# Optimization experiments

Hardware: AMD Instinct MI355X
Metric: run time of the kernel (lower is better)

## Reference

```python
import jax, jax.numpy as jnp
import numpy as np

EMBED_DIM = 1024
ATTEN_DIM = 64


def setup_inputs() -> dict:
    key = jax.random.key(0)
    k_x, k_q, k_k, k_v = jax.random.split(key, 4)
    B, S = 4, 4096
    scale = 1.0 / np.sqrt(EMBED_DIM)
    x = jax.random.normal(k_x, (B, S, EMBED_DIM), dtype=jnp.float32)
    # torch nn.Linear weights are [out_features, in_features]
    Wq = jax.random.normal(k_q, (ATTEN_DIM, EMBED_DIM), dtype=jnp.float32) * scale
    Wk = jax.random.normal(k_k, (ATTEN_DIM, EMBED_DIM), dtype=jnp.float32) * scale
    Wv = jax.random.normal(k_v, (ATTEN_DIM, EMBED_DIM), dtype=jnp.float32) * scale
    return {"x": x, "Wq": Wq, "Wk": Wk, "Wv": Wv}


def reference(x, Wq, Wk, Wv):
    # q, k, v: [B, S, D]
    q = jnp.einsum('bse,de->bsd', x, Wq)
    k = jnp.einsum('bse,de->bsd', x, Wk)
    v = jnp.einsum('bse,de->bsd', x, Wv)
    d = k.shape[-1]
    scores = jnp.einsum('bsd,btd->bst', q, k) / jnp.sqrt(jnp.float32(d))
    S = x.shape[1]
    causal = jnp.tril(jnp.ones((S, S), dtype=bool))
    scores = jnp.where(causal[None, :, :], scores, -jnp.inf)
    attn = jax.nn.softmax(scores, axis=-1)
    return jnp.einsum('bst,btd->bsd', attn, v)
```

## Files before the change

### kernel.cpp

```cpp
#include <hip/hip_runtime.h>
#include <hip/hip_bf16.h>
#include <stdint.h>

typedef __attribute__((ext_vector_type(8))) short  short8;
typedef __attribute__((ext_vector_type(4))) short  short4v;
typedef __attribute__((ext_vector_type(4))) float  float4v;

#define MFMA16(a, b, c) __builtin_amdgcn_mfma_f32_16x16x32_bf16((a), (b), (c), 0, 0, 0)

#define S_LEN  4096
#define NBATCH 4
#define EMB    1024
#define DD     64
#define NROWS  (NBATCH * S_LEN)
#define SCL2   0.1803368801111204f

static __device__ __forceinline__ short f2bf(float f) {
  uint32_t u = __float_as_uint(f);
  return (short)((u + 0x7FFFu + ((u >> 16) & 1u)) >> 16);
}
static __device__ __forceinline__ unsigned pk2(float a, float b) {
  union { __hip_bfloat162 h; unsigned u; } z;
  z.h = __float22bfloat162_rn(make_float2(a, b));
  return z.u;
}
static __device__ __forceinline__ short8 cvt8(float4v a, float4v b) {
  union { unsigned u[4]; short8 s; } z;
  z.u[0] = pk2(a[0], a[1]); z.u[1] = pk2(a[2], a[3]);
  z.u[2] = pk2(b[0], b[1]); z.u[3] = pk2(b[2], b[3]);
  return z.s;
}

__global__ void wcvt_kernel(const float* __restrict__ Wq, const float* __restrict__ Wk,
                            const float* __restrict__ Wv, short* __restrict__ Wb2) {
  const int t   = blockIdx.x * 256 + threadIdx.x;
  const int row = t >> 7;
  const int k   = (t & 127) * 8;
  const float* src = (row < 64) ? (Wq + (size_t)row * EMB)
                   : (row < 128) ? (Wk + (size_t)(row - 64) * EMB)
                                 : (Wv + (size_t)(row - 128) * EMB);
  const float sc = (row < 64) ? SCL2 : 1.0f;
  float4v a = *(const float4v*)(src + k);
  float4v b = *(const float4v*)(src + k + 4);
#pragma unroll
  for (int i = 0; i < 4; ++i) { a[i] *= sc; b[i] *= sc; }
  *(short8*)(Wb2 + (((k >> 5) * 192 + row) << 5) + (k & 31)) = cvt8(a, b);
}

__global__ __launch_bounds__(256, 4) void qkv_kernel(
    const float* __restrict__ x, const short* __restrict__ Wb2,
    short* __restrict__ Qb, short* __restrict__ Kb, short* __restrict__ Vt) {
  const int tid  = threadIdx.x;
  const int w    = tid >> 6;
  const int lane = tid & 63;
  const int ln   = lane & 15;
  const int quad = lane >> 4;
  const int m0   = blockIdx.x * 16;

  const float* xp = x + (size_t)(m0 + ln) * EMB + quad * 8;
  const short* wp[3];
#pragma unroll
  for (int i = 0; i < 3; ++i)
    wp[i] = Wb2 + (size_t)(i * 64 + w * 16 + ln) * 32 + quad * 8;

  const float4v zz = {0.f, 0.f, 0.f, 0.f};
  float4v acc[3] = {zz, zz, zz};

  float4v a0[2], a1[2];
  short8 bpf[2][3];
#pragma unroll
  for (int s = 0; s < 2; ++s) {
    a0[s] = *(const float4v*)(xp + s * 32);
    a1[s] = *(const float4v*)(xp + s * 32 + 4);
#pragma unroll
    for (int i = 0; i < 3; ++i)
      bpf[s][i] = *(const short8*)(wp[i] + (size_t)s * 6144);
  }

  for (int s = 0; s < 32; ++s) {
    const int cur = s & 1;
    const short8 xf = cvt8(a0[cur], a1[cur]);
    short8 bf[3];
#pragma unroll
    for (int i = 0; i < 3; ++i) bf[i] = bpf[cur][i];
    const int sn = (s + 2 < 32) ? s + 2 : s;
    a0[cur] = *(const float4v*)(xp + sn * 32);
    a1[cur] = *(const float4v*)(xp + sn * 32 + 4);
#pragma unroll
    for (int i = 0; i < 3; ++i)
      bpf[cur][i] = *(const short8*)(wp[i] + (size_t)sn * 6144);
    acc[0] = MFMA16(xf, bf[0], acc[0]);
    acc[1] = MFMA16(xf, bf[1], acc[1]);
    acc[2] = MFMA16(bf[2], xf, acc[2]);
  }

  const int b  = m0 >> 12;
  const int sb = m0 & (S_LEN - 1);
#pragma unroll
  for (int r = 0; r < 4; ++r) {
    const int row = m0 + quad * 4 + r;
    Qb[(size_t)row * DD + w * 16 + ln] = f2bf(acc[0][r]);
    Kb[(size_t)row * DD + w * 16 + ln] = f2bf(acc[1][r]);
    const int d = w * 16 + quad * 4 + r;
    Vt[((size_t)b * DD + d) * S_LEN + sb + ln] = f2bf(acc[2][r]);
  }
}

#define PSTRW 76

__global__ __launch_bounds__(512, 2) void attn_kernel(
    const short* __restrict__ Qb, const short* __restrict__ Kb,
    const short* __restrict__ Vt, float* __restrict__ out) {
  __shared__ float sbuf[8][32 * PSTRW];
  __shared__ float llds[8][32];

  const int tid  = threadIdx.x;
  const int w    = tid >> 6;
  const int lane = tid & 63;
  const int ln   = lane & 15;
  const int quad = lane >> 4;
  const int g    = blockIdx.x;
  const int b    = g & 3;
  const int j    = g >> 2;
  const short* Kbase = Kb + (size_t)b * S_LEN * DD;
  const short* Vbase = Vt + (size_t)b * DD * S_LEN;
  float* pw = &sbuf[w][0];
  const float4v zz = {0.f, 0.f, 0.f, 0.f};

  for (int ph = 0; ph < 2; ++ph) {
    const int band = ph ? (127 - j) : j;
    const int qb   = band * 32;
    const int qg0  = b * S_LEN + qb;

    short8 aQ[2][2];
#pragma unroll
    for (int rfi = 0; rfi < 2; ++rfi)
#pragma unroll
      for (int h = 0; h < 2; ++h)
        aQ[rfi][h] = *(const short8*)(Qb + (size_t)(qg0 + rfi * 16 + ln) * DD + h * 32 + quad * 8);

    float4v o[2][4];
    float lp[2][4];
#pragma unroll
    for (int rfi = 0; rfi < 2; ++rfi)
#pragma unroll
      for (int d = 0; d < 4; ++d) { o[rfi][d] = zz; lp[rfi][d] = 0.f; }

    const int T = (qb + 95) >> 6;

    short8 Kc[4][2], Kn[4][2];
#pragma unroll
    for (int c = 0; c < 4; ++c)
#pragma unroll
      for (int h = 0; h < 2; ++h)
        Kc[c][h] = *(const short8*)(Kbase + (size_t)(w * 64 + c * 16 + ln) * DD + h * 32 + quad * 8);

    for (int it = w; it < T; it += 8) {
      const int kv0 = it * 64;
      short8 Vc[4][2];
#pragma unroll
      for (int d = 0; d < 4; ++d)
#pragma unroll
        for (int h = 0; h < 2; ++h)
          Vc[d][h] = *(const short8*)(Vbase + (size_t)(d * 16 + ln) * S_LEN + kv0 + h * 32 + quad * 8);

      float4v s[2][4];
#pragma unroll
      for (int rfi = 0; rfi < 2; ++rfi)
#pragma unroll
        for (int c = 0; c < 4; ++c) {
          s[rfi][c] = MFMA16(aQ[rfi][0], Kc[c][0], zz);
          s[rfi][c] = MFMA16(aQ[rfi][1], Kc[c][1], s[rfi][c]);
        }

      const int kvn = (it + 8 < T) ? (it + 8) * 64 : 0;
#pragma unroll
      for (int c = 0; c < 4; ++c)
#pragma unroll
        for (int h = 0; h < 2; ++h)
          Kn[c][h] = *(const short8*)(Kbase + (size_t)(kvn + c * 16 + ln) * DD + h * 32 + quad * 8);

      const bool needmask = (kv0 + 63) > qb;
#pragma unroll
      for (int rfi = 0; rfi < 2; ++rfi) {
        float p[4][4];
#pragma unroll
        for (int c = 0; c < 4; ++c)
#pragma unroll
          for (int r = 0; r < 4; ++r) {
            float e = exp2f(fminf(s[rfi][c][r], 60.0f));
            if (needmask && (kv0 + c * 16 + ln > qb + rfi * 16 + quad * 4 + r)) e = 0.f;
            p[c][r] = e;
          }
#pragma unroll
        for (int r = 0; r < 4; ++r)
          lp[rfi][r] += p[0][r] + p[1][r] + p[2][r] + p[3][r];
#pragma unroll
        for (int c = 0; c < 4; ++c)
#pragma unroll
          for (int r = 0; r < 4; ++r)
            pw[(rfi * 16 + quad * 4 + r) * PSTRW + c * 16 + ln] = p[c][r];
      }
      asm volatile("s_waitcnt lgkmcnt(0)" ::: "memory");
      short8 aP[2][2];
#pragma unroll
      for (int rfi = 0; rfi < 2; ++rfi)
#pragma unroll
        for (int h = 0; h < 2; ++h) {
          const float4v lo = *(const float4v*)&pw[(rfi * 16 + ln) * PSTRW + h * 32 + quad * 8];
          const float4v hi = *(const float4v*)&pw[(rfi * 16 + ln) * PSTRW + h * 32 + quad * 8 + 4];
          aP[rfi][h] = cvt8(lo, hi);
        }
#pragma unroll
      for (int rfi = 0; rfi < 2; ++rfi)
#pragma unroll
        for (int d = 0; d < 4; ++d) {
          o[rfi][d] = MFMA16(aP[rfi][0], Vc[d][0], o[rfi][d]);
          o[rfi][d] = MFMA16(aP[rfi][1], Vc[d][1], o[rfi][d]);
        }
#pragma unroll
      for (int c = 0; c < 4; ++c)
#pragma unroll
        for (int h = 0; h < 2; ++h)
          Kc[c][h] = Kn[c][h];
    }

#pragma unroll
    for (int rfi = 0; rfi < 2; ++rfi)
#pragma unroll
      for (int r = 0; r < 4; ++r) {
        float lr = lp[rfi][r];
        lr += __shfl_xor(lr, 1);
        lr += __shfl_xor(lr, 2);
        lr += __shfl_xor(lr, 4);
        lr += __shfl_xor(lr, 8);
        if (ln == 0) llds[w][rfi * 16 + quad * 4 + r] = lr;
#pragma unroll
        for (int d = 0; d < 4; ++d)
          pw[(rfi * 16 + quad * 4 + r) * 64 + d * 16 + ln] = o[rfi][d][r];
      }
    __syncthreads();

#pragma unroll
    for (int jj = 0; jj < 4; ++jj) {
      const int idx = tid + jj * 512;
      const int row = idx >> 6, col = idx & 63;
      float sum = 0.f, lt = 0.f;
#pragma unroll
      for (int wi = 0; wi < 8; ++wi) {
        sum += sbuf[wi][row * 64 + col];
        lt  += llds[wi][row];
      }
      out[(size_t)(qg0 + row) * DD + col] = sum / lt;
    }
    __syncthreads();
  }
}

extern "C" void kernel_launch(void* const* d_in, const int* in_sizes, int n_in,
                              void* d_out, int out_size, void* d_ws, size_t ws_size,
                              hipStream_t stream) {
  const float* x  = (const float*)d_in[0];
  const float* Wq = (const float*)d_in[1];
  const float* Wk = (const float*)d_in[2];
  const float* Wv = (const float*)d_in[3];

  short* Qb  = (short*)d_ws;
  short* Kb  = Qb + (size_t)NROWS * DD;
  short* Vt  = Kb + (size_t)NROWS * DD;
  short* Wb2 = Vt + (size_t)NROWS * DD;

  wcvt_kernel<<<dim3(96), dim3(256), 0, stream>>>(Wq, Wk, Wv, Wb2);
  qkv_kernel<<<dim3(NROWS / 16), dim3(256), 0, stream>>>(x, Wb2, Qb, Kb, Vt);
  attn_kernel<<<dim3(NBATCH * 64), dim3(512), 0, stream>>>(Qb, Kb, Vt, (float*)d_out);
}
```

Before: 181.5 us.

## Stage QKV projection tiles in LDS via async global-to-LDS loads

The QKV projection kernel now processes 32 rows per block instead of 16. It stages x and the packed weights into double-buffered shared memory using global_load_lds direct copies. Each wave computes six 16x16 output fragments from LDS, so weight reuse rises and each block issues fewer redundant weight reads. This adds __syncthreads per K-step, about 64KB of LDS per block, and lower occupancy (launch bounds 2). The ordering of the LDS buffers relies on the barrier placement.

After: 161.5 us. 1.12x faster.

```diff
diff --git a/kernel.cpp b/kernel.cpp
--- a/kernel.cpp
+++ b/kernel.cpp
@@ -14,6 +14,9 @@
 #define DD     64
 #define NROWS  (NBATCH * S_LEN)
 #define SCL2   0.1803368801111204f
+
+#define AS1 const __attribute__((address_space(1))) unsigned int*
+#define AS3 __attribute__((address_space(3))) unsigned int*
 
 static __device__ __forceinline__ short f2bf(float f) {
   uint32_t u = __float_as_uint(f);
@@ -47,62 +50,98 @@
   *(short8*)(Wb2 + (((k >> 5) * 192 + row) << 5) + (k & 31)) = cvt8(a, b);
 }
 
-__global__ __launch_bounds__(256, 4) void qkv_kernel(
+__global__ __launch_bounds__(256, 2) void qkv_kernel(
     const float* __restrict__ x, const short* __restrict__ Wb2,
     short* __restrict__ Qb, short* __restrict__ Kb, short* __restrict__ Vt) {
+  __shared__ float As[2][2048];
+  __shared__ short Bs[2][12288];
+
   const int tid  = threadIdx.x;
   const int w    = tid >> 6;
   const int lane = tid & 63;
   const int ln   = lane & 15;
   const int quad = lane >> 4;
-  const int m0   = blockIdx.x * 16;
-
-  const float* xp = x + (size_t)(m0 + ln) * EMB + quad * 8;
-  const short* wp[3];
-#pragma unroll
-  for (int i = 0; i < 3; ++i)
-    wp[i] = Wb2 + (size_t)(i * 64 + w * 16 + ln) * 32 + quad * 8;
+  const int m0   = blockIdx.x * 32;
+  const int wr   = w & 1;
+  const int wc   = w >> 1;
+
+  const int tA0 = 2 * w, tA1 = 2 * w + 1;
+  const float* xA0 = x + (size_t)(m0 + ((tA0 >> 2) << 4) + (lane >> 2)) * EMB
+                       + ((tA0 & 3) * 4 + (lane & 3)) * 4;
+  const float* xA1 = x + (size_t)(m0 + ((tA1 >> 2) << 4) + (lane >> 2)) * EMB
+                       + ((tA1 & 3) * 4 + (lane & 3)) * 4;
+  const short* wB = Wb2 + (size_t)(6 * w) * 512 + lane * 8;
+
+#define STAGE(S, BUF) do {                                                      \
+    __builtin_amdgcn_global_load_lds((AS1)(xA0 + (S) * 64),                     \
+        (AS3)&As[BUF][tA0 * 256], 16, 0, 0);                                    \
+    __builtin_amdgcn_global_load_lds((AS1)(xA1 + (S) * 64),                     \
+        (AS3)&As[BUF][tA1 * 256], 16, 0, 0);                                    \
+    _Pragma("unroll")                                                           \
+    for (int j = 0; j < 6; ++j)                                                 \
+      __builtin_amdgcn_global_load_lds((AS1)(wB + (size_t)(S) * 12288 + j * 512),\
+          (AS3)&Bs[BUF][(6 * w + j) * 512], 16, 0, 0);                          \
+  } while (0)
 
   const float4v zz = {0.f, 0.f, 0.f, 0.f};
-  float4v acc[3] = {zz, zz, zz};
-
-  float4v a0[2], a1[2];
-  short8 bpf[2][3];
-#pragma unroll
-  for (int s = 0; s < 2; ++s) {
-    a0[s] = *(const float4v*)(xp + s * 32);
-    a1[s] = *(const float4v*)(xp + s * 32 + 4);
-#pragma unroll
-    for (int i = 0; i < 3; ++i)
-      bpf[s][i] = *(const short8*)(wp[i] + (size_t)s * 6144);
+  float4v acc[6] = {zz, zz, zz, zz, zz, zz};
+
+  STAGE(0, 0);
+  int buf = 0;
+  for (int s = 0; s < 16; ++s) {
+    __syncthreads();
+    if (s + 1 < 16) STAGE(s + 1, buf ^ 1);
+    short8 aF[2];
+#pragma unroll
+    for (int h = 0; h < 2; ++h) {
+      const int ai = (wr * 4 + 2 * h + (quad >> 1)) * 256 + (ln * 4 + (quad & 1) * 2) * 4;
+      const float4v lo = *(const float4v*)&As[buf][ai];
+      const float4v hi = *(const float4v*)&As[buf][ai + 4];
+      aF[h] = cvt8(lo, hi);
+    }
+#pragma unroll
+    for (int f = 0; f < 6; ++f) {
+      const int cf = wc * 6 + f;
+      const short8 b0 = *(const short8*)&Bs[buf][(cf * 16 + ln) * 32 + quad * 8];
+      const short8 b1 = *(const short8*)&Bs[buf][6144 + (cf * 16 + ln) * 32 + quad * 8];
+      if (wc == 0 || f < 2) {
+        acc[f] = MFMA16(aF[0], b0, acc[f]);
+        acc[f] = MFMA16(aF[1], b1, acc[f]);
+      } else {
+        acc[f] = MFMA16(b0, aF[0], acc[f]);
+        acc[f] = MFMA16(b1, aF[1], acc[f]);
+      }
+    }
+    buf ^= 1;
   }
-
-  for (int s = 0; s < 32; ++s) {
-    const int cur = s & 1;
-    const short8 xf = cvt8(a0[cur], a1[cur]);
-    short8 bf[3];
-#pragma unroll
-    for (int i = 0; i < 3; ++i) bf[i] = bpf[cur][i];
-    const int sn = (s + 2 < 32) ? s + 2 : s;
-    a0[cur] = *(const float4v*)(xp + sn * 32);
-    a1[cur] = *(const float4v*)(xp + sn * 32 + 4);
-#pragma unroll
-    for (int i = 0; i < 3; ++i)
-      bpf[cur][i] = *(const short8*)(wp[i] + (size_t)sn * 6144);
-    acc[0] = MFMA16(xf, bf[0], acc[0]);
-    acc[1] = MFMA16(xf, bf[1], acc[1]);
-    acc[2] = MFMA16(bf[2], xf, acc[2]);
-  }
+#undef STAGE
 
   const int b  = m0 >> 12;
   const int sb = m0 & (S_LEN - 1);
-#pragma unroll
-  for (int r = 0; r < 4; ++r) {
-    const int row = m0 + quad * 4 + r;
-    Qb[(size_t)row * DD + w * 16 + ln] = f2bf(acc[0][r]);
-    Kb[(size_t)row * DD + w * 16 + ln] = f2bf(acc[1][r]);
-    const int d = w * 16 + quad * 4 + r;
-    Vt[((size_t)b * DD + d) * S_LEN + sb + ln] = f2bf(acc[2][r]);
+  if (wc == 0) {
+#pragma unroll
+    for (int f = 0; f < 6; ++f)
+#pragma unroll
+      for (int r = 0; r < 4; ++r) {
+        const int row = m0 + wr * 16 + quad * 4 + r;
+        if (f < 4) Qb[(size_t)row * DD + f * 16 + ln] = f2bf(acc[f][r]);
+        else       Kb[(size_t)row * DD + (f - 4) * 16 + ln] = f2bf(acc[f][r]);
+      }
+  } else {
+#pragma unroll
+    for (int f = 0; f < 2; ++f)
+#pragma unroll
+      for (int r = 0; r < 4; ++r) {
+        const int row = m0 + wr * 16 + quad * 4 + r;
+        Kb[(size_t)row * DD + 32 + f * 16 + ln] = f2bf(acc[f][r]);
+      }
+#pragma unroll
+    for (int f = 2; f < 6; ++f)
+#pragma unroll
+      for (int r = 0; r < 4; ++r) {
+        const int d = (f - 2) * 16 + quad * 4 + r;
+        Vt[((size_t)b * DD + d) * S_LEN + sb + wr * 16 + ln] = f2bf(acc[f][r]);
+      }
   }
 }
 
@@ -271,6 +310,6 @@
   short* Wb2 = Vt + (size_t)NROWS * DD;
 
   wcvt_kernel<<<dim3(96), dim3(256), 0, stream>>>(Wq, Wk, Wv, Wb2);
-  qkv_kernel<<<dim3(NROWS / 16), dim3(256), 0, stream>>>(x, Wb2, Qb, Kb, Vt);
+  qkv_kernel<<<dim3(NROWS / 32), dim3(256), 0, stream>>>(x, Wb2, Qb, Kb, Vt);
   attn_kernel<<<dim3(NBATCH * 64), dim3(512), 0, stream>>>(Qb, Kb, Vt, (float*)d_out);
 }
```
